# Kernel tuning notes

Hardware: AMD Instinct MI355X
Metric: run time of the kernel (lower is better)

The kernel has to match this reference:

```python
import jax, jax.numpy as jnp
import numpy as np

D_MODEL = 1024
N_HEADS = 16


def setup_inputs() -> dict:
    key = jax.random.key(0)
    k1, k2, k3 = jax.random.split(key, 3)
    x = jax.random.normal(k1, (4, 2048, D_MODEL), dtype=jnp.float32)
    # torch nn.Linear(D, 3D): weight (3D, D), bias (3D)
    W = jax.random.normal(k2, (3 * D_MODEL, D_MODEL), dtype=jnp.float32) * (D_MODEL ** -0.5)
    b = jax.random.normal(k3, (3 * D_MODEL,), dtype=jnp.float32) * 0.01
    return {"x": x, "W": W, "b": b}


def reference(x, W, b):
    N, C, D = x.shape
    H = N_HEADS
    hd = D // H
    z = jnp.einsum("ncd,ed->nce", x, W) + b  # [N, C, 3D]
    k = z[:, :, :D].reshape(N, C, H, hd).transpose(0, 2, 1, 3)
    q = z[:, :, D:2 * D].reshape(N, C, H, hd).transpose(0, 2, 1, 3)
    v = z[:, :, 2 * D:].reshape(N, C, H, hd).transpose(0, 2, 1, 3)
    # NOTE: original scales by full model dim D, not head dim
    scores = jnp.einsum("nhqd,nhkd->nhqk", q, k) * (D ** -0.5)
    causal = jnp.tril(jnp.ones((C, C), dtype=bool))
    scores = jnp.where(causal[None, None], scores, -jnp.inf)
    attn = jax.nn.softmax(scores, axis=-1)
    out = jnp.einsum("nhqk,nhkd->nhqd", attn, v)
    return out.transpose(0, 2, 1, 3).reshape(N, C, D)
```

## Files before the change

kernel.cpp:

```cpp
#include <hip/hip_runtime.h>
#include <hip/hip_bf16.h>

typedef __bf16 bf16;
typedef __bf16 bf16x8 __attribute__((ext_vector_type(8)));
typedef float f32x4 __attribute__((ext_vector_type(4)));
typedef unsigned int u32x4 __attribute__((ext_vector_type(4)));

#define SEQ   2048
#define NBAT  4
#define DM    1024
#define NH    16
#define HD    64
#define E3    3072

__global__ void cvt2_bf16_kernel(const float* __restrict__ a, bf16* __restrict__ oa, int na8,
                                 const float* __restrict__ b, bf16* __restrict__ ob, int nb8) {
  const int stride = gridDim.x * blockDim.x;
  const int ntot = na8 + nb8;
  for (int i = blockIdx.x * blockDim.x + threadIdx.x; i < ntot; i += stride) {
    const float* src;
    bf16* dst;
    int j;
    if (i < na8) { src = a; dst = oa; j = i; }
    else         { src = b; dst = ob; j = i - na8; }
    const float4* p = (const float4*)(src + (size_t)j * 8);
    float4 x = p[0];
    float4 y = p[1];
    bf16x8 o;
    o[0] = (bf16)x.x; o[1] = (bf16)x.y; o[2] = (bf16)x.z; o[3] = (bf16)x.w;
    o[4] = (bf16)y.x; o[5] = (bf16)y.y; o[6] = (bf16)y.z; o[7] = (bf16)y.w;
    *(bf16x8*)(dst + (size_t)j * 8) = o;
  }
}

#define BM 128
#define BN 128
#define BK 32
#define KSTEPS (DM / BK)

__global__ __launch_bounds__(256, 2) void qkv_gemm_kernel(
    const bf16* __restrict__ A, const bf16* __restrict__ B,
    const float* __restrict__ bias, bf16* __restrict__ Z)
{
  __shared__ bf16 sA[2][BM * BK];
  __shared__ bf16 sB[2][BN * BK];

  const int tid  = threadIdx.x;
  const int lane = tid & 63;
  const int w    = tid >> 6;
  const int wr   = w >> 1;
  const int wc   = w & 1;
  const int m0   = blockIdx.x * BM;
  const int n0   = blockIdx.y * BN;

  const f32x4 z4 = {0.f, 0.f, 0.f, 0.f};
  f32x4 acc[4][4];
#pragma unroll
  for (int i = 0; i < 4; ++i)
#pragma unroll
    for (int j = 0; j < 4; ++j)
      acc[i][j] = z4;

  const int srow = w * 32 + (lane >> 2);
  const int skk  = (lane & 3) * 8;
  const bf16* gA = A + (size_t)m0 * DM;
  const bf16* gB = B + (size_t)n0 * DM;

  auto stage = [&](int buf, int t) {
    const int k0 = t * BK;
#pragma unroll
    for (int c = 0; c < 2; ++c)
      __builtin_amdgcn_global_load_lds(
          (const __attribute__((address_space(1))) unsigned int*)(gA + (size_t)(srow + c * 16) * DM + k0 + skk),
          (__attribute__((address_space(3))) unsigned int*)(&sA[buf][w * 1024 + c * 512]),
          16, 0, 0);
#pragma unroll
    for (int c = 0; c < 2; ++c)
      __builtin_amdgcn_global_load_lds(
          (const __attribute__((address_space(1))) unsigned int*)(gB + (size_t)(srow + c * 16) * DM + k0 + skk),
          (__attribute__((address_space(3))) unsigned int*)(&sB[buf][w * 1024 + c * 512]),
          16, 0, 0);
  };

  stage(0, 0);
  int cur = 0;
  const int arow = wr * 64 + (lane & 15);
  const int brow = wc * 64 + (lane & 15);
  const int kf   = (lane >> 4) * 8;

  for (int t = 0; t < KSTEPS; ++t) {
    __syncthreads();
    if (t + 1 < KSTEPS) stage(cur ^ 1, t + 1);
    bf16x8 af[4], bfr[4];
#pragma unroll
    for (int i = 0; i < 4; ++i)
      af[i] = *(const bf16x8*)&sA[cur][(arow + i * 16) * BK + kf];
#pragma unroll
    for (int j = 0; j < 4; ++j)
      bfr[j] = *(const bf16x8*)&sB[cur][(brow + j * 16) * BK + kf];
#pragma unroll
    for (int i = 0; i < 4; ++i)
#pragma unroll
      for (int j = 0; j < 4; ++j)
        acc[i][j] = __builtin_amdgcn_mfma_f32_16x16x32_bf16(af[i], bfr[j], acc[i][j], 0, 0, 0);
    cur ^= 1;
  }

#pragma unroll
  for (int i = 0; i < 4; ++i) {
#pragma unroll
    for (int j = 0; j < 4; ++j) {
      const int col = n0 + wc * 64 + j * 16 + (lane & 15);
      const float bb = bias[col];
#pragma unroll
      for (int r = 0; r < 4; ++r) {
        const int row = m0 + wr * 64 + i * 16 + (lane >> 4) * 4 + r;
        Z[(size_t)row * E3 + col] = (bf16)(acc[i][j][r] + bb);
      }
    }
  }
}

#define QB 64
#define KB 64
#define NQT (SEQ / QB)

__global__ __launch_bounds__(256, 4) void attn_kernel(
    const bf16* __restrict__ Z, float* __restrict__ out)
{
  __shared__ bf16 sK[2][KB][64];
  __shared__ bf16 sVT[2][HD][64];

  const int tid   = threadIdx.x;
  const int lane  = tid & 63;
  const int w     = tid >> 6;
  const int l15   = lane & 15;
  const int lhi   = lane >> 4;
  const int l7    = l15 & 7;
  const int e2    = l15 >> 3;

  const int flat = blockIdx.x + 16 * (blockIdx.y + 16 * blockIdx.z);
  const int v    = (flat & 7) * 128 + (flat >> 3);
  const int bx   = v & 15;
  const int h    = (v >> 4) & 15;
  const int n    = v >> 8;

  const size_t zb = (size_t)n * SEQ * E3;
  const int kcol0 = h * HD;
  const int qcol0 = DM + h * HD;
  const int vcol0 = 2 * DM + h * HD;

  const f32x4 z4 = {0.f, 0.f, 0.f, 0.f};
  const f32x4 neg4 = {-1e32f, -1e32f, -1e32f, -1e32f};
  const float scale = 0.03125f;
  const float L2E   = 1.4426950408889634f;
  const float SL2E  = scale * L2E;
  const float DEFER = 4.0f;

  const u32x4 onesu = {0x3F803F80u, 0x3F803F80u, 0x3F803F80u, 0x3F803F80u};
  const bf16x8 onesf = __builtin_bit_cast(bf16x8, onesu);

  const int c0row = tid >> 3;
  const int t7    = tid & 7;
  const int c0col = t7 * 8;
  const int sgk = ((c0row & 12) << 1) | ((c0row & 16) >> 2) | (c0row & 3);

  const int krow_in = lane >> 3;
  const int kdblk   = ((lane & 7) ^ (lane >> 3)) * 8;

  const size_t ob = (size_t)n * SEQ * DM;

  bf16x8 vpre[2];
  auto vload = [&](int t) {
#pragma unroll
    for (int c = 0; c < 2; ++c)
      vpre[c] = *(const bf16x8*)&Z[zb + (size_t)(t * KB + c0row + 32 * c) * E3 + vcol0 + c0col];
  };
  auto lwriteV = [&](int buf) {
#pragma unroll
    for (int c = 0; c < 2; ++c)
#pragma unroll
      for (int j = 0; j < 8; ++j)
        sVT[buf][c0col + j][(sgk + 32 * c) ^ ((j ^ t7) << 3)] = vpre[c][j];
  };
  auto stageK = [&](int t, int buf) {
#pragma unroll
    for (int c = 0; c < 2; ++c) {
      const int cc = 2 * w + c;
      __builtin_amdgcn_global_load_lds(
          (const __attribute__((address_space(1))) unsigned int*)(
              Z + zb + (size_t)(t * KB + 8 * cc + krow_in) * E3 + kcol0 + kdblk),
          (__attribute__((address_space(3))) unsigned int*)(&sK[buf][8 * cc][0]),
          16, 0, 0);
    }
  };

#pragma unroll 1
  for (int phase = 0; phase < 2; ++phase) {
    const int qtile = phase == 0 ? bx : (NQT - 1 - bx);
    const int qwave = qtile * QB + w * 16;
    const int T     = qtile + 1;

    bf16x8 qf[2];
    {
      const int qrow = qwave + l15;
#pragma unroll
      for (int kk = 0; kk < 2; ++kk)
        qf[kk] = *(const bf16x8*)&Z[zb + (size_t)qrow * E3 + qcol0 + kk * 32 + lhi * 8];
    }

    f32x4 accO[4];
    f32x4 accL;
#pragma unroll
    for (int dt = 0; dt < 4; ++dt) accO[dt] = z4;
    accL = z4;
    float mrow = -1e30f;

    stageK(0, 0);
    vload(0);
    lwriteV(0);
    if (T > 1) vload(1);
    __syncthreads();

#pragma unroll 1
    for (int t = 0; t < T; ++t) {
      const int cur = t & 1;
      if (t + 1 < T) { stageK(t + 1, cur ^ 1); lwriteV(cur ^ 1); }
      if (t + 2 < T) vload(t + 2);

      f32x4 st[4];
      __builtin_amdgcn_s_setprio(1);
#pragma unroll
      for (int kt = 0; kt < 4; ++kt) {
        const int blk0 = (lhi ^ l7) * 8;
        const int blk1 = ((4 + lhi) ^ l7) * 8;
        bf16x8 kf0 = *(const bf16x8*)&sK[cur][kt * 16 + l15][blk0];
        st[kt] = __builtin_amdgcn_mfma_f32_16x16x32_bf16(kf0, qf[0], z4, 0, 0, 0);
        bf16x8 kf1 = *(const bf16x8*)&sK[cur][kt * 16 + l15][blk1];
        st[kt] = __builtin_amdgcn_mfma_f32_16x16x32_bf16(kf1, qf[1], st[kt], 0, 0, 0);
      }
      __builtin_amdgcn_s_setprio(0);

      if (t == T - 1) {
#pragma unroll
        for (int kt = 0; kt < 4; ++kt) {
          if (kt > w) st[kt] = neg4;
          else if (kt == w) {
#pragma unroll
            for (int r = 0; r < 4; ++r)
              if (lhi * 4 + r > l15) st[kt][r] = -1e32f;
          }
        }
      }

      float a0 = fmaxf(fmaxf(st[0][0], st[0][1]), st[0][2]);
      float a1 = fmaxf(fmaxf(st[0][3], st[1][0]), st[1][1]);
      float a2 = fmaxf(fmaxf(st[1][2], st[1][3]), st[2][0]);
      float a3 = fmaxf(fmaxf(st[2][1], st[2][2]), st[2][3]);
      float a4 = fmaxf(fmaxf(st[3][0], st[3][1]), st[3][2]);
      float b0 = fmaxf(fmaxf(a0, a1), a2);
      float b1 = fmaxf(fmaxf(a3, a4), st[3][3]);
      float mr = fmaxf(b0, b1);
      mr = fmaxf(mr, __shfl_xor(mr, 16));
      mr = fmaxf(mr, __shfl_xor(mr, 32));
      const float mxs = mr * scale;

      if (__any(mxs > mrow + DEFER)) {
        const float mnew  = fmaxf(mrow, mxs);
        const float alpha = exp2f((mrow - mnew) * L2E);
        mrow = mnew;
#pragma unroll
        for (int dt = 0; dt < 4; ++dt) accO[dt] *= alpha;
        accL *= alpha;
      }

      const float mm = -mrow * L2E;
      bf16x8 pb[2];
#pragma unroll
      for (int c = 0; c < 2; ++c) {
        u32x4 pu;
#pragma unroll
        for (int i = 0; i < 4; ++i) {
          const int kt = 2 * c + (i >> 1);
          const int r  = (2 * i) & 3;
          const float p0 = exp2f(fmaf(st[kt][r],     SL2E, mm));
          const float p1 = exp2f(fmaf(st[kt][r + 1], SL2E, mm));
          const bf16 b0v = (bf16)p0;
          const bf16 b1v = (bf16)p1;
          pu[i] = (unsigned int)__builtin_bit_cast(unsigned short, b0v)
                | ((unsigned int)__builtin_bit_cast(unsigned short, b1v) << 16);
        }
        pb[c] = __builtin_bit_cast(bf16x8, pu);
      }

      __builtin_amdgcn_s_setprio(1);
#pragma unroll
      for (int c = 0; c < 2; ++c)
        accL = __builtin_amdgcn_mfma_f32_16x16x32_bf16(onesf, pb[c], accL, 0, 0, 0);

#pragma unroll
      for (int c = 0; c < 2; ++c) {
#pragma unroll
        for (int dt = 0; dt < 4; ++dt) {
          const int idx = ((4 * c + lhi) ^ (l7 ^ ((2 * dt + e2) & 7))) << 3;
          const bf16x8 av = *(const bf16x8*)&sVT[cur][dt * 16 + l15][idx];
          accO[dt] = __builtin_amdgcn_mfma_f32_16x16x32_bf16(av, pb[c], accO[dt], 0, 0, 0);
        }
      }
      __builtin_amdgcn_s_setprio(0);

      __syncthreads();
    }

    {
      const float inv  = 1.f / accL[0];
      const int   qrow = qwave + l15;
#pragma unroll
      for (int dt = 0; dt < 4; ++dt) {
        float4 o;
        o.x = accO[dt][0] * inv;
        o.y = accO[dt][1] * inv;
        o.z = accO[dt][2] * inv;
        o.w = accO[dt][3] * inv;
        *(float4*)&out[ob + (size_t)qrow * DM + h * HD + dt * 16 + lhi * 4] = o;
      }
    }
  }
}

extern "C" void kernel_launch(void* const* d_in, const int* in_sizes, int n_in,
                              void* d_out, int out_size, void* d_ws, size_t ws_size,
                              hipStream_t stream) {
  const float* x    = (const float*)d_in[0];
  const float* W    = (const float*)d_in[1];
  const float* bias = (const float*)d_in[2];
  float* out = (float*)d_out;

  bf16* xb = (bf16*)d_ws;
  bf16* Wb = xb + (size_t)NBAT * SEQ * DM;
  bf16* Zb = Wb + (size_t)E3 * DM;

  cvt2_bf16_kernel<<<1536, 256, 0, stream>>>(x, xb, NBAT * SEQ * DM / 8,
                                             W, Wb, E3 * DM / 8);

  dim3 g1(NBAT * SEQ / BM, E3 / BN);
  qkv_gemm_kernel<<<g1, 256, 0, stream>>>(xb, Wb, bias, Zb);

  dim3 g2(NQT / 2, NH, NBAT);
  attn_kernel<<<g2, 256, 0, stream>>>(Zb, out);
}
```

Before: 161.2 us.

## Speculatively compute softmax exps before max reduction and relax loop barrier waits

Computes the exponentials with the previous running max before the row-max reduction, recomputing them only when the max update branch is taken. This moves exp work off the critical path after the cross-lane shuffles. The end-of-iteration barrier now uses a partial vmcnt wait, and the V prefetch is always issued (clamped index) so the counter count stays fixed. This lets global loads remain in flight across the barrier. The cost is doubled exp work when the rescale happens and a fragile hand-counted waitcnt.

After: 173.8 us. +7.9%, slower.

```diff
diff --git a/kernel.cpp b/kernel.cpp
--- a/kernel.cpp
+++ b/kernel.cpp
@@ -226,7 +226,8 @@
     for (int t = 0; t < T; ++t) {
       const int cur = t & 1;
       if (t + 1 < T) { stageK(t + 1, cur ^ 1); lwriteV(cur ^ 1); }
-      if (t + 2 < T) vload(t + 2);
+      asm volatile("" ::: "memory");
+      if (t + 1 < T) vload(t + 2 < T ? t + 2 : T - 1);
 
       f32x4 st[4];
       __builtin_amdgcn_s_setprio(1);
@@ -252,6 +253,25 @@
           }
         }
       }
+
+      u32x4 pu[2];
+      {
+        const float mm = -mrow * L2E;
+#pragma unroll
+        for (int c = 0; c < 2; ++c)
+#pragma unroll
+          for (int i = 0; i < 4; ++i) {
+            const int kt = 2 * c + (i >> 1);
+            const int r  = (2 * i) & 3;
+            const float p0 = exp2f(fmaf(st[kt][r],     SL2E, mm));
+            const float p1 = exp2f(fmaf(st[kt][r + 1], SL2E, mm));
+            const bf16 b0v = (bf16)p0;
+            const bf16 b1v = (bf16)p1;
+            pu[c][i] = (unsigned int)__builtin_bit_cast(unsigned short, b0v)
+                     | ((unsigned int)__builtin_bit_cast(unsigned short, b1v) << 16);
+          }
+      }
+      asm volatile("" : "+v"(pu[0]), "+v"(pu[1]));
 
       float a0 = fmaxf(fmaxf(st[0][0], st[0][1]), st[0][2]);
       float a1 = fmaxf(fmaxf(st[0][3], st[1][0]), st[1][1]);
@@ -272,44 +292,47 @@
 #pragma unroll
         for (int dt = 0; dt < 4; ++dt) accO[dt] *= alpha;
         accL *= alpha;
-      }
-
-      const float mm = -mrow * L2E;
-      bf16x8 pb[2];
+        const float mm = -mrow * L2E;
+#pragma unroll
+        for (int c = 0; c < 2; ++c)
+#pragma unroll
+          for (int i = 0; i < 4; ++i) {
+            const int kt = 2 * c + (i >> 1);
+            const int r  = (2 * i) & 3;
+            const float p0 = exp2f(fmaf(st[kt][r],     SL2E, mm));
+            const float p1 = exp2f(fmaf(st[kt][r + 1], SL2E, mm));
+            const bf16 b0v = (bf16)p0;
+            const bf16 b1v = (bf16)p1;
+            pu[c][i] = (unsigned int)__builtin_bit_cast(unsigned short, b0v)
+                     | ((unsigned int)__builtin_bit_cast(unsigned short, b1v) << 16);
+          }
+      }
+      const bf16x8 pb0 = __builtin_bit_cast(bf16x8, pu[0]);
+      const bf16x8 pb1 = __builtin_bit_cast(bf16x8, pu[1]);
+
+      __builtin_amdgcn_s_setprio(1);
+      accL = __builtin_amdgcn_mfma_f32_16x16x32_bf16(onesf, pb0, accL, 0, 0, 0);
+      accL = __builtin_amdgcn_mfma_f32_16x16x32_bf16(onesf, pb1, accL, 0, 0, 0);
+
 #pragma unroll
       for (int c = 0; c < 2; ++c) {
-        u32x4 pu;
-#pragma unroll
-        for (int i = 0; i < 4; ++i) {
-          const int kt = 2 * c + (i >> 1);
-          const int r  = (2 * i) & 3;
-          const float p0 = exp2f(fmaf(st[kt][r],     SL2E, mm));
-          const float p1 = exp2f(fmaf(st[kt][r + 1], SL2E, mm));
-          const bf16 b0v = (bf16)p0;
-          const bf16 b1v = (bf16)p1;
-          pu[i] = (unsigned int)__builtin_bit_cast(unsigned short, b0v)
-                | ((unsigned int)__builtin_bit_cast(unsigned short, b1v) << 16);
-        }
-        pb[c] = __builtin_bit_cast(bf16x8, pu);
-      }
-
-      __builtin_amdgcn_s_setprio(1);
-#pragma unroll
-      for (int c = 0; c < 2; ++c)
-        accL = __builtin_amdgcn_mfma_f32_16x16x32_bf16(onesf, pb[c], accL, 0, 0, 0);
-
-#pragma unroll
-      for (int c = 0; c < 2; ++c) {
+        const bf16x8 pbc = c ? pb1 : pb0;
 #pragma unroll
         for (int dt = 0; dt < 4; ++dt) {
           const int idx = ((4 * c + lhi) ^ (l7 ^ ((2 * dt + e2) & 7))) << 3;
           const bf16x8 av = *(const bf16x8*)&sVT[cur][dt * 16 + l15][idx];
-          accO[dt] = __builtin_amdgcn_mfma_f32_16x16x32_bf16(av, pb[c], accO[dt], 0, 0, 0);
+          accO[dt] = __builtin_amdgcn_mfma_f32_16x16x32_bf16(av, pbc, accO[dt], 0, 0, 0);
         }
       }
       __builtin_amdgcn_s_setprio(0);
 
-      __syncthreads();
+      if (t + 1 < T) {
+        asm volatile("s_waitcnt vmcnt(2) lgkmcnt(0)" ::: "memory");
+        __builtin_amdgcn_s_barrier();
+        asm volatile("" ::: "memory");
+      } else {
+        __syncthreads();
+      }
     }
 
     {
```

## Halve attention KV tile, one q-tile per block, remap grid for balance

Applied to the files above, without the earlier changes.

The attention kernel now uses 32-key tiles instead of 64, and each block handles one query tile instead of a paired short/long phase. The grid becomes a flat 2048-block launch with a remapped ordering that interleaves short and long causal tiles. Shared memory per block is halved and launch bounds are raised to allow more resident blocks per CU. The intent is higher occupancy and finer load balancing. The cost is twice as many loop iterations with a barrier each, and less MFMA work per barrier.

After: 173.3 us. 7.5% more time.

```diff
diff --git a/kernel.cpp b/kernel.cpp
--- a/kernel.cpp
+++ b/kernel.cpp
@@ -122,14 +122,14 @@
 }
 
 #define QB 64
-#define KB 64
+#define KB 32
 #define NQT (SEQ / QB)
 
-__global__ __launch_bounds__(256, 4) void attn_kernel(
+__global__ __launch_bounds__(256, 8) void attn_kernel(
     const bf16* __restrict__ Z, float* __restrict__ out)
 {
   __shared__ bf16 sK[2][KB][64];
-  __shared__ bf16 sVT[2][HD][64];
+  __shared__ bf16 sVT[2][HD][KB];
 
   const int tid   = threadIdx.x;
   const int lane  = tid & 63;
@@ -139,11 +139,15 @@
   const int l7    = l15 & 7;
   const int e2    = l15 >> 3;
 
-  const int flat = blockIdx.x + 16 * (blockIdx.y + 16 * blockIdx.z);
-  const int v    = (flat & 7) * 128 + (flat >> 3);
-  const int bx   = v & 15;
-  const int h    = (v >> 4) & 15;
-  const int n    = v >> 8;
+  const int flat  = blockIdx.x;
+  const int s     = flat & 255;
+  const int j     = flat >> 8;
+  const int ctx   = s & 63;
+  const int qslot = s >> 6;
+  const int p     = j >> 1;
+  const int qtile = (j & 1) ? (NQT - 1 - (qslot * 4 + p)) : (qslot * 4 + p);
+  const int h     = ctx & 15;
+  const int n     = ctx >> 4;
 
   const size_t zb = (size_t)n * SEQ * E3;
   const int kcol0 = h * HD;
@@ -170,160 +174,140 @@
 
   const size_t ob = (size_t)n * SEQ * DM;
 
-  bf16x8 vpre[2];
+  bf16x8 vpre;
   auto vload = [&](int t) {
-#pragma unroll
-    for (int c = 0; c < 2; ++c)
-      vpre[c] = *(const bf16x8*)&Z[zb + (size_t)(t * KB + c0row + 32 * c) * E3 + vcol0 + c0col];
+    vpre = *(const bf16x8*)&Z[zb + (size_t)(t * KB + c0row) * E3 + vcol0 + c0col];
   };
   auto lwriteV = [&](int buf) {
 #pragma unroll
-    for (int c = 0; c < 2; ++c)
-#pragma unroll
-      for (int j = 0; j < 8; ++j)
-        sVT[buf][c0col + j][(sgk + 32 * c) ^ ((j ^ t7) << 3)] = vpre[c][j];
+    for (int jj = 0; jj < 8; ++jj)
+      sVT[buf][c0col + jj][sgk ^ ((((jj ^ t7) & 3)) << 3)] = vpre[jj];
   };
   auto stageK = [&](int t, int buf) {
-#pragma unroll
-    for (int c = 0; c < 2; ++c) {
-      const int cc = 2 * w + c;
-      __builtin_amdgcn_global_load_lds(
-          (const __attribute__((address_space(1))) unsigned int*)(
-              Z + zb + (size_t)(t * KB + 8 * cc + krow_in) * E3 + kcol0 + kdblk),
-          (__attribute__((address_space(3))) unsigned int*)(&sK[buf][8 * cc][0]),
-          16, 0, 0);
-    }
+    __builtin_amdgcn_global_load_lds(
+        (const __attribute__((address_space(1))) unsigned int*)(
+            Z + zb + (size_t)(t * KB + 8 * w + krow_in) * E3 + kcol0 + kdblk),
+        (__attribute__((address_space(3))) unsigned int*)(&sK[buf][8 * w][0]),
+        16, 0, 0);
   };
 
+  const int qwave = qtile * QB + w * 16;
+  const int T     = 2 * (qtile + 1);
+  const int dg    = 4 * qtile + w;
+
+  bf16x8 qf[2];
+  {
+    const int qrow = qwave + l15;
+#pragma unroll
+    for (int kk = 0; kk < 2; ++kk)
+      qf[kk] = *(const bf16x8*)&Z[zb + (size_t)qrow * E3 + qcol0 + kk * 32 + lhi * 8];
+  }
+
+  f32x4 accO[4];
+  f32x4 accL;
+#pragma unroll
+  for (int dt = 0; dt < 4; ++dt) accO[dt] = z4;
+  accL = z4;
+  float mrow = -1e30f;
+
+  stageK(0, 0);
+  vload(0);
+  lwriteV(0);
+  vload(1);
+  __syncthreads();
+
 #pragma unroll 1
-  for (int phase = 0; phase < 2; ++phase) {
-    const int qtile = phase == 0 ? bx : (NQT - 1 - bx);
-    const int qwave = qtile * QB + w * 16;
-    const int T     = qtile + 1;
-
-    bf16x8 qf[2];
-    {
-      const int qrow = qwave + l15;
-#pragma unroll
-      for (int kk = 0; kk < 2; ++kk)
-        qf[kk] = *(const bf16x8*)&Z[zb + (size_t)qrow * E3 + qcol0 + kk * 32 + lhi * 8];
-    }
-
-    f32x4 accO[4];
-    f32x4 accL;
-#pragma unroll
-    for (int dt = 0; dt < 4; ++dt) accO[dt] = z4;
-    accL = z4;
-    float mrow = -1e30f;
-
-    stageK(0, 0);
-    vload(0);
-    lwriteV(0);
-    if (T > 1) vload(1);
-    __syncthreads();
-
-#pragma unroll 1
-    for (int t = 0; t < T; ++t) {
-      const int cur = t & 1;
-      if (t + 1 < T) { stageK(t + 1, cur ^ 1); lwriteV(cur ^ 1); }
-      if (t + 2 < T) vload(t + 2);
-
-      f32x4 st[4];
-      __builtin_amdgcn_s_setprio(1);
-#pragma unroll
-      for (int kt = 0; kt < 4; ++kt) {
-        const int blk0 = (lhi ^ l7) * 8;
-        const int blk1 = ((4 + lhi) ^ l7) * 8;
-        bf16x8 kf0 = *(const bf16x8*)&sK[cur][kt * 16 + l15][blk0];
-        st[kt] = __builtin_amdgcn_mfma_f32_16x16x32_bf16(kf0, qf[0], z4, 0, 0, 0);
-        bf16x8 kf1 = *(const bf16x8*)&sK[cur][kt * 16 + l15][blk1];
-        st[kt] = __builtin_amdgcn_mfma_f32_16x16x32_bf16(kf1, qf[1], st[kt], 0, 0, 0);
-      }
-      __builtin_amdgcn_s_setprio(0);
-
-      if (t == T - 1) {
-#pragma unroll
-        for (int kt = 0; kt < 4; ++kt) {
-          if (kt > w) st[kt] = neg4;
-          else if (kt == w) {
-#pragma unroll
-            for (int r = 0; r < 4; ++r)
-              if (lhi * 4 + r > l15) st[kt][r] = -1e32f;
-          }
+  for (int t = 0; t < T; ++t) {
+    const int cur = t & 1;
+    if (t + 1 < T) { stageK(t + 1, cur ^ 1); lwriteV(cur ^ 1); }
+    if (t + 2 < T) vload(t + 2);
+
+    f32x4 st[2];
+    __builtin_amdgcn_s_setprio(1);
+#pragma unroll
+    for (int kt = 0; kt < 2; ++kt) {
+      const int blk0 = (lhi ^ l7) * 8;
+      const int blk1 = ((4 + lhi) ^ l7) * 8;
+      bf16x8 kf0 = *(const bf16x8*)&sK[cur][kt * 16 + l15][blk0];
+      st[kt] = __builtin_amdgcn_mfma_f32_16x16x32_bf16(kf0, qf[0], z4, 0, 0, 0);
+      bf16x8 kf1 = *(const bf16x8*)&sK[cur][kt * 16 + l15][blk1];
+      st[kt] = __builtin_amdgcn_mfma_f32_16x16x32_bf16(kf1, qf[1], st[kt], 0, 0, 0);
+    }
+    __builtin_amdgcn_s_setprio(0);
+
+    if (2 * t + 1 >= dg) {
+#pragma unroll
+      for (int kt = 0; kt < 2; ++kt) {
+        const int fg = 2 * t + kt;
+        if (fg > dg) st[kt] = neg4;
+        else if (fg == dg) {
+#pragma unroll
+          for (int r = 0; r < 4; ++r)
+            if (lhi * 4 + r > l15) st[kt][r] = -1e32f;
         }
       }
-
-      float a0 = fmaxf(fmaxf(st[0][0], st[0][1]), st[0][2]);
-      float a1 = fmaxf(fmaxf(st[0][3], st[1][0]), st[1][1]);
-      float a2 = fmaxf(fmaxf(st[1][2], st[1][3]), st[2][0]);
-      float a3 = fmaxf(fmaxf(st[2][1], st[2][2]), st[2][3]);
-      float a4 = fmaxf(fmaxf(st[3][0], st[3][1]), st[3][2]);
-      float b0 = fmaxf(fmaxf(a0, a1), a2);
-      float b1 = fmaxf(fmaxf(a3, a4), st[3][3]);
-      float mr = fmaxf(b0, b1);
-      mr = fmaxf(mr, __shfl_xor(mr, 16));
-      mr = fmaxf(mr, __shfl_xor(mr, 32));
-      const float mxs = mr * scale;
-
-      if (__any(mxs > mrow + DEFER)) {
-        const float mnew  = fmaxf(mrow, mxs);
-        const float alpha = exp2f((mrow - mnew) * L2E);
-        mrow = mnew;
-#pragma unroll
-        for (int dt = 0; dt < 4; ++dt) accO[dt] *= alpha;
-        accL *= alpha;
+    }
+
+    float a0 = fmaxf(fmaxf(st[0][0], st[0][1]), st[0][2]);
+    float a1 = fmaxf(fmaxf(st[0][3], st[1][0]), st[1][1]);
+    float a2 = fmaxf(st[1][2], st[1][3]);
+    float mr = fmaxf(fmaxf(a0, a1), a2);
+    mr = fmaxf(mr, __shfl_xor(mr, 16));
+    mr = fmaxf(mr, __shfl_xor(mr, 32));
+    const float mxs = mr * scale;
+
+    if (__any(mxs > mrow + DEFER)) {
+      const float mnew  = fmaxf(mrow, mxs);
+      const float alpha = exp2f((mrow - mnew) * L2E);
+      mrow = mnew;
+#pragma unroll
+      for (int dt = 0; dt < 4; ++dt) accO[dt] *= alpha;
+      accL *= alpha;
+    }
+
+    const float mm = -mrow * L2E;
+    bf16x8 pb;
+    {
+      u32x4 pu;
+#pragma unroll
+      for (int i = 0; i < 4; ++i) {
+        const int kt = i >> 1;
+        const int r  = (2 * i) & 3;
+        const float p0 = exp2f(fmaf(st[kt][r],     SL2E, mm));
+        const float p1 = exp2f(fmaf(st[kt][r + 1], SL2E, mm));
+        const bf16 b0v = (bf16)p0;
+        const bf16 b1v = (bf16)p1;
+        pu[i] = (unsigned int)__builtin_bit_cast(unsigned short, b0v)
+              | ((unsigned int)__builtin_bit_cast(unsigned short, b1v) << 16);
       }
-
-      const float mm = -mrow * L2E;
-      bf16x8 pb[2];
-#pragma unroll
-      for (int c = 0; c < 2; ++c) {
-        u32x4 pu;
-#pragma unroll
-        for (int i = 0; i < 4; ++i) {
-          const int kt = 2 * c + (i >> 1);
-          const int r  = (2 * i) & 3;
-          const float p0 = exp2f(fmaf(st[kt][r],     SL2E, mm));
-          const float p1 = exp2f(fmaf(st[kt][r + 1], SL2E, mm));
-          const bf16 b0v = (bf16)p0;
-          const bf16 b1v = (bf16)p1;
-          pu[i] = (unsigned int)__builtin_bit_cast(unsigned short, b0v)
-                | ((unsigned int)__builtin_bit_cast(unsigned short, b1v) << 16);
-        }
-        pb[c] = __builtin_bit_cast(bf16x8, pu);
-      }
-
-      __builtin_amdgcn_s_setprio(1);
-#pragma unroll
-      for (int c = 0; c < 2; ++c)
-        accL = __builtin_amdgcn_mfma_f32_16x16x32_bf16(onesf, pb[c], accL, 0, 0, 0);
-
-#pragma unroll
-      for (int c = 0; c < 2; ++c) {
-#pragma unroll
-        for (int dt = 0; dt < 4; ++dt) {
-          const int idx = ((4 * c + lhi) ^ (l7 ^ ((2 * dt + e2) & 7))) << 3;
-          const bf16x8 av = *(const bf16x8*)&sVT[cur][dt * 16 + l15][idx];
-          accO[dt] = __builtin_amdgcn_mfma_f32_16x16x32_bf16(av, pb[c], accO[dt], 0, 0, 0);
-        }
-      }
-      __builtin_amdgcn_s_setprio(0);
-
-      __syncthreads();
-    }
-
-    {
-      const float inv  = 1.f / accL[0];
-      const int   qrow = qwave + l15;
-#pragma unroll
-      for (int dt = 0; dt < 4; ++dt) {
-        float4 o;
-        o.x = accO[dt][0] * inv;
-        o.y = accO[dt][1] * inv;
-        o.z = accO[dt][2] * inv;
-        o.w = accO[dt][3] * inv;
-        *(float4*)&out[ob + (size_t)qrow * DM + h * HD + dt * 16 + lhi * 4] = o;
-      }
+      pb = __builtin_bit_cast(bf16x8, pu);
+    }
+
+    __builtin_amdgcn_s_setprio(1);
+    accL = __builtin_amdgcn_mfma_f32_16x16x32_bf16(onesf, pb, accL, 0, 0, 0);
+
+#pragma unroll
+    for (int dt = 0; dt < 4; ++dt) {
+      const int idx = (lhi ^ ((l7 ^ (2 * dt + e2)) & 3)) << 3;
+      const bf16x8 av = *(const bf16x8*)&sVT[cur][dt * 16 + l15][idx];
+      accO[dt] = __builtin_amdgcn_mfma_f32_16x16x32_bf16(av, pb, accO[dt], 0, 0, 0);
+    }
+    __builtin_amdgcn_s_setprio(0);
+
+    __syncthreads();
+  }
+
+  {
+    const float inv  = 1.f / accL[0];
+    const int   qrow = qwave + l15;
+#pragma unroll
+    for (int dt = 0; dt < 4; ++dt) {
+      float4 o;
+      o.x = accO[dt][0] * inv;
+      o.y = accO[dt][1] * inv;
+      o.z = accO[dt][2] * inv;
+      o.w = accO[dt][3] * inv;
+      *(float4*)&out[ob + (size_t)qrow * DM + h * HD + dt * 16 + lhi * 4] = o;
     }
   }
 }
@@ -346,6 +330,5 @@
   dim3 g1(NBAT * SEQ / BM, E3 / BN);
   qkv_gemm_kernel<<<g1, 256, 0, stream>>>(xb, Wb, bias, Zb);
 
-  dim3 g2(NQT / 2, NH, NBAT);
-  attn_kernel<<<g2, 256, 0, stream>>>(Zb, out);
+  attn_kernel<<<2048, 256, 0, stream>>>(Zb, out);
 }
```
